# Optimization experiments

Hardware: AMD Instinct MI355X
Metric: run time of the kernel (lower is better)

Reference implementation:

```python
import jax, jax.numpy as jnp
import numpy as np

D_INPUT = 1024
N_HEADS = 16
D_INNER = 64
SEQ = 1024
PREV = 1024
BS = 4
LN_EPS = 1e-5


def _rel_shift(x):
    # x: (i, j, b, h) -> Transformer-XL relative shift trick
    i, j, b, h = x.shape
    zero_pad = jnp.zeros((i, 1, b, h), dtype=x.dtype)
    return jnp.concatenate([zero_pad, x], axis=1).reshape(j + 1, i, b, h)[1:].reshape(i, j, b, h)


def setup_inputs() -> dict:
    key = jax.random.key(0)
    ks = jax.random.split(key, 9)
    w = 0.02
    return {
        "input_": jax.random.normal(ks[0], (SEQ, BS, D_INPUT), jnp.float32),
        "pos_embs": jax.random.normal(ks[1], (SEQ + PREV, D_INPUT), jnp.float32),
        "memory": jax.random.normal(ks[2], (PREV, BS, D_INPUT), jnp.float32),
        "u": jax.random.normal(ks[3], (N_HEADS, D_INNER), jnp.float32) * w,
        "v": jax.random.normal(ks[4], (N_HEADS, D_INNER), jnp.float32) * w,
        "W_kv": jax.random.normal(ks[5], (D_INPUT, 2 * N_HEADS * D_INNER), jnp.float32) * w,
        "W_q": jax.random.normal(ks[6], (D_INPUT, N_HEADS * D_INNER), jnp.float32) * w,
        "W_p": jax.random.normal(ks[7], (D_INPUT, N_HEADS * D_INNER), jnp.float32) * w,
        "W_out": jax.random.normal(ks[8], (N_HEADS * D_INNER, D_INPUT), jnp.float32) * w,
        "ln_g": jnp.ones((D_INPUT,), jnp.float32),
        "ln_b": jnp.zeros((D_INPUT,), jnp.float32),
    }


def reference(input_, pos_embs, memory, u, v, W_kv, W_q, W_p, W_out, ln_g, ln_b):
    S, B, D = input_.shape
    P = memory.shape[0]
    T = S + P
    H, d = u.shape
    scale = 1.0 / (d ** 0.5)

    x_mem = jnp.concatenate([memory, input_], axis=0)          # (T, B, D)
    kv = x_mem @ W_kv                                          # (T, B, 2*H*d)
    k, val = jnp.split(kv, 2, axis=-1)
    k = k.reshape(T, B, H, d)
    val = val.reshape(T, B, H, d)
    q = (input_ @ W_q).reshape(S, B, H, d)                     # (S, B, H, d)

    content_attn = jnp.einsum('ibhd,jbhd->ijbh', q + u, k)     # (S, T, B, H)
    p = (pos_embs @ W_p).reshape(T, H, d)                      # (T, H, d)
    position_attn = jnp.einsum('ibhd,jhd->ijbh', q + v, p)     # (S, T, B, H)
    position_attn = _rel_shift(position_attn)

    attn = jax.nn.softmax((content_attn + position_attn) * scale, axis=1)
    awv = jnp.einsum('ijbh,jbhd->ibhd', attn, val).reshape(S, B, H * d)

    out = input_ + awv @ W_out                                 # residual
    mu = jnp.mean(out, axis=-1, keepdims=True)
    var = jnp.mean(jnp.square(out - mu), axis=-1, keepdims=True)
    return (out - mu) * jax.lax.rsqrt(var + LN_EPS) * ln_g + ln_b
```

## Files before the change

kernel.cpp:

```cpp
#include <hip/hip_runtime.h>
#include <cstdint>
#include <cstddef>

#define S_  1024
#define B_  4
#define T_  2048
#define H_  16

typedef short     short8 __attribute__((ext_vector_type(8)));
typedef float     f32x4  __attribute__((ext_vector_type(4)));
typedef unsigned short u16x8 __attribute__((ext_vector_type(8)));

__device__ __forceinline__ unsigned short f2b(float f){
  uint32_t x = __builtin_bit_cast(uint32_t, f);
  x = (x + 0x7fffu + ((x >> 16) & 1u)) >> 16;
  return (unsigned short)x;
}
__device__ __forceinline__ unsigned short f2bt(float f){
  return (unsigned short)(__builtin_bit_cast(uint32_t, f) >> 16);
}
__device__ __forceinline__ float b2f(unsigned short u){
  return __builtin_bit_cast(float, ((uint32_t)u) << 16);
}

__device__ __forceinline__ void gl_lds16(const unsigned short* g, unsigned short* l){
  __builtin_amdgcn_global_load_lds(
      (const __attribute__((address_space(1))) void*)g,
      (__attribute__((address_space(3))) void*)l,
      16, 0, 0);
}

__global__ __launch_bounds__(256) void cvt_all(
    const float* __restrict__ memsrc, const float* __restrict__ inp,
    const float* __restrict__ pos,
    unsigned short* __restrict__ xb, unsigned short* __restrict__ posb)
{
  int i = (blockIdx.x * 256 + threadIdx.x) * 4;
  const float* src;
  unsigned short* dst;
  if (i < 8192 * 1024){
    src = (i < 4096 * 1024) ? (memsrc + i) : (inp + (i - 4096 * 1024));
    dst = xb + i;
  } else {
    int i2 = i - 8192 * 1024;
    src = pos + i2;
    dst = posb + i2;
  }
  float4 x = *(const float4*)src;
  ushort4 o;
  o.x = f2b(x.x); o.y = f2b(x.y); o.z = f2b(x.z); o.w = f2b(x.w);
  *(ushort4*)dst = o;
}

__global__ __launch_bounds__(256) void wtrans_all(
    const float* __restrict__ Wkv, const float* __restrict__ Wq,
    const float* __restrict__ Wp,  const float* __restrict__ Wout,
    unsigned short* __restrict__ WkvT, unsigned short* __restrict__ WqT,
    unsigned short* __restrict__ WpT,  unsigned short* __restrict__ WoutT)
{
  __shared__ float tile[32][33];
  int blk = blockIdx.x;
  const float* in; unsigned short* out; int C, bx, by;
  if (blk < 2048){ in = Wkv; out = WkvT; C = 2048; bx = blk & 63; by = blk >> 6; }
  else {
    int r = blk - 2048; int wi = r >> 10; r &= 1023;
    C = 1024; bx = r & 31; by = r >> 5;
    in  = (wi == 0) ? Wq  : ((wi == 1) ? Wp  : Wout);
    out = (wi == 0) ? WqT : ((wi == 1) ? WpT : WoutT);
  }
  const int R0 = by * 32, C0 = bx * 32;
  const int t = threadIdx.x;
  const int r = t >> 3, c4 = (t & 7) * 4;
  float4 x = *(const float4*)(in + (size_t)(R0 + r) * C + C0 + c4);
  tile[r][c4+0] = x.x; tile[r][c4+1] = x.y; tile[r][c4+2] = x.z; tile[r][c4+3] = x.w;
  __syncthreads();
  ushort4 o;
  o.x = f2b(tile[c4+0][r]); o.y = f2b(tile[c4+1][r]);
  o.z = f2b(tile[c4+2][r]); o.w = f2b(tile[c4+3][r]);
  *(ushort4*)(out + (size_t)(C0 + r) * 1024 + R0 + c4) = o;
}

__global__ __launch_bounds__(256) void vtrans(
    const unsigned short* __restrict__ kvb, unsigned short* __restrict__ vtg)
{
  __shared__ __align__(16) unsigned short tile[64][72];
  const int t = threadIdx.x;
  const int bh = blockIdx.y;
  const int b = bh >> 4, h = bh & 15;
  const int t0 = blockIdx.x * 64;
  #pragma unroll
  for (int l = 0; l < 2; ++l){
    int idx = t + l * 256;
    int row = idx >> 3, seg = (idx & 7) * 8;
    u16x8 x = *(const u16x8*)(kvb + ((size_t)(t0 + row) * 4 + b) * 2048 + 1024 + h * 64 + seg);
    *(u16x8*)&tile[row][seg] = x;
  }
  __syncthreads();
  #pragma unroll
  for (int l = 0; l < 2; ++l){
    int idx = t + l * 256;
    int d = idx >> 3, nseg = (idx & 7) * 8;
    u16x8 o;
    #pragma unroll
    for (int j = 0; j < 8; ++j) o[j] = tile[nseg + j][d];
    *(u16x8*)(vtg + ((size_t)bh * 64 + d) * 2048 + t0 + nseg) = o;
  }
}

#define AS_IDX(row,k) ((((row) >> 3) * 512) + (((k) >> 3) * 64) + (((row) & 7) * 8) + ((k) & 7))

__global__ __launch_bounds__(256) void gemm_multi(
    const unsigned short* __restrict__ xb,
    const unsigned short* __restrict__ posb,
    const unsigned short* __restrict__ WkvT,
    const unsigned short* __restrict__ WqT,
    const unsigned short* __restrict__ WpT,
    unsigned short* __restrict__ kvb,
    unsigned short* __restrict__ qbb,
    unsigned short* __restrict__ pbb)
{
  const unsigned short *A, *BT;
  unsigned short* C;
  int N, local;
  int bx = (blockIdx.x & 7) * 176 + (blockIdx.x >> 3);
  if (bx < 1024){       A = xb;                       BT = WkvT; C = kvb; N = 2048; local = bx;        }
  else if (bx < 1280){  A = xb + (size_t)4096 * 1024; BT = WqT;  C = qbb; N = 1024; local = bx - 1024; }
  else {                A = posb;                     BT = WpT;  C = pbb; N = 1024; local = bx - 1280; }
  const int nb = N >> 7;
  const int M0 = (local / nb) * 128, N0 = (local % nb) * 128;
  const int K = 1024;

  __shared__ __align__(16) unsigned short As[128 * 64];
  __shared__ __align__(16) unsigned short Bs[128 * 64];
  const int t = threadIdx.x;
  const int w = t >> 6, lane = t & 63, quad = lane >> 4, l16 = lane & 15;
  const int wm = (w >> 1) * 64, wn = (w & 1) * 64;
  const int lr = lane & 7, lcb = lane >> 3;

  f32x4 acc[4][4] = {};

  for (int k0 = 0; k0 < K; k0 += 64){
    __syncthreads();
    #pragma unroll
    for (int i = 0; i < 4; ++i){
      int blk = 4 * w + i;
      gl_lds16(A  + (size_t)(M0 + 8 * blk + lr) * K + k0 + lcb * 8, As + blk * 512);
      gl_lds16(BT + (size_t)(N0 + 8 * blk + lr) * K + k0 + lcb * 8, Bs + blk * 512);
    }
    __syncthreads();
    #pragma unroll
    for (int ks = 0; ks < 2; ++ks){
      short8 af[4], bf[4];
      #pragma unroll
      for (int rt = 0; rt < 4; ++rt)
        af[rt] = *(short8*)&As[AS_IDX(wm + rt * 16 + l16, ks * 32 + quad * 8)];
      #pragma unroll
      for (int ct = 0; ct < 4; ++ct)
        bf[ct] = *(short8*)&Bs[AS_IDX(wn + ct * 16 + l16, ks * 32 + quad * 8)];
      #pragma unroll
      for (int rt = 0; rt < 4; ++rt)
        #pragma unroll
        for (int ct = 0; ct < 4; ++ct)
          acc[rt][ct] = __builtin_amdgcn_mfma_f32_16x16x32_bf16(af[rt], bf[ct], acc[rt][ct], 0, 0, 0);
    }
  }

  #pragma unroll
  for (int rt = 0; rt < 4; ++rt)
    #pragma unroll
    for (int r = 0; r < 4; ++r){
      int row = M0 + wm + rt * 16 + quad * 4 + r;
      #pragma unroll
      for (int ct = 0; ct < 4; ++ct)
        C[(size_t)row * N + N0 + wn + ct * 16 + l16] = f2b(acc[rt][ct][r]);
    }
}

__global__ __launch_bounds__(256) void gemm_outk(
    const unsigned short* __restrict__ A,
    const unsigned short* __restrict__ BT,
    float* __restrict__ OutP)
{
  const int K = 1024, N = 1024;
  int lid = blockIdx.x + 8 * (blockIdx.y + 32 * blockIdx.z);
  int sw  = (lid & 7) * 64 + (lid >> 3);
  const int N0 = (sw & 7) * 128;
  const int M0 = ((sw >> 3) & 31) * 128;
  const int kz = sw >> 8;
  const int k0s = kz * 512, k0e = k0s + 512;
  float* outF = OutP + (size_t)kz * 4096 * 1024;

  __shared__ __align__(16) unsigned short As[128 * 64];
  __shared__ __align__(16) unsigned short Bs[128 * 64];
  const int t = threadIdx.x;
  const int w = t >> 6, lane = t & 63, quad = lane >> 4, l16 = lane & 15;
  const int wm = (w >> 1) * 64, wn = (w & 1) * 64;
  const int lr = lane & 7, lcb = lane >> 3;

  f32x4 acc[4][4] = {};

  for (int k0 = k0s; k0 < k0e; k0 += 64){
    __syncthreads();
    #pragma unroll
    for (int i = 0; i < 4; ++i){
      int blk = 4 * w + i;
      gl_lds16(A  + (size_t)(M0 + 8 * blk + lr) * K + k0 + lcb * 8, As + blk * 512);
      gl_lds16(BT + (size_t)(N0 + 8 * blk + lr) * K + k0 + lcb * 8, Bs + blk * 512);
    }
    __syncthreads();
    #pragma unroll
    for (int ks = 0; ks < 2; ++ks){
      short8 af[4], bf[4];
      #pragma unroll
      for (int rt = 0; rt < 4; ++rt)
        af[rt] = *(short8*)&As[AS_IDX(wm + rt * 16 + l16, ks * 32 + quad * 8)];
      #pragma unroll
      for (int ct = 0; ct < 4; ++ct)
        bf[ct] = *(short8*)&Bs[AS_IDX(wn + ct * 16 + l16, ks * 32 + quad * 8)];
      #pragma unroll
      for (int rt = 0; rt < 4; ++rt)
        #pragma unroll
        for (int ct = 0; ct < 4; ++ct)
          acc[rt][ct] = __builtin_amdgcn_mfma_f32_16x16x32_bf16(af[rt], bf[ct], acc[rt][ct], 0, 0, 0);
    }
  }

  #pragma unroll
  for (int rt = 0; rt < 4; ++rt)
    #pragma unroll
    for (int r = 0; r < 4; ++r){
      int row = M0 + wm + rt * 16 + quad * 4 + r;
      #pragma unroll
      for (int ct = 0; ct < 4; ++ct)
        outF[(size_t)row * N + N0 + wn + ct * 16 + l16] = acc[rt][ct][r];
    }
}

#define SP_IX(gm,n) ((gm) * 64 + ((n) ^ (((gm) & 12) << 2)))

__global__ __launch_bounds__(256, 3) void attn_mfma(
    const unsigned short* __restrict__ qb,
    const unsigned short* __restrict__ kvb,
    const unsigned short* __restrict__ pbm,
    const unsigned short* __restrict__ vtg,
    const float* __restrict__ ub, const float* __restrict__ vb,
    unsigned short* __restrict__ opart,
    float* __restrict__ lpart)
{
  __shared__ __align__(16) unsigned short Kc[64 * 64];
  __shared__ __align__(16) unsigned short VT[64 * 64];
  __shared__ __align__(16) unsigned short Pw[128 * 64];
  __shared__ __align__(16) unsigned short SP[64 * 64];

  const int t = threadIdx.x;
  const int i0 = blockIdx.x * 64;
  const int bh = blockIdx.y;
  const int jh = blockIdx.z;
  const int b = bh >> 4, h = bh & 15;
  const int w = t >> 6, lane = t & 63, quad = lane >> 4, l16 = lane & 15;
  const int colbase = h * 64 + quad * 8;
  const int ctLo = 3 - w;

  const float SCQ = 0.1803368801f;
  const float EOF_ = 23.0831206f;

  short8 qu[2], qv[2][2];
  #pragma unroll
  for (int cs = 0; cs < 2; ++cs){
    int gr = i0 + 16 * w + l16 + cs;
    #pragma unroll
    for (int ks = 0; ks < 2; ++ks){
      u16x8 q8 = *(const u16x8*)(qb + ((size_t)gr * 4 + b) * 1024 + colbase + ks * 32);
      #pragma unroll
      for (int j = 0; j < 8; ++j){
        float f = b2f(q8[j]);
        qv[cs][ks][j] = (short)f2b((f + vb[colbase + ks * 32 + j]) * SCQ);
        if (cs == 0) qu[ks][j] = (short)f2b((f + ub[colbase + ks * 32 + j]) * SCQ);
      }
    }
  }

  f32x4 oacc[4] = {};
  float lsum[4] = {0.f, 0.f, 0.f, 0.f};

  u16x8 pk[2], pv2[2], pp[4];

  auto loadKV = [&](int jc){
    const int j0 = jc * 64;
    #pragma unroll
    for (int l = 0; l < 2; ++l){
      int idx = t + l * 256;
      int row = idx >> 3, cb = idx & 7;
      pk[l]  = *(const u16x8*)(kvb + ((size_t)(j0 + row) * 4 + b) * 2048 + h * 64 + cb * 8);
      pv2[l] = *(const u16x8*)(vtg + ((size_t)bh * 64 + row) * 2048 + j0 + cb * 8);
    }
  };

  auto loadPPfull = [&](int jc){
    const int D = jc * 64 - i0;
    #pragma unroll
    for (int l = 0; l < 4; ++l){
      int idx = t + l * 256;
      int row = idx >> 3, cb = idx & 7;
      int pr;
      if (D <= 960)          pr = D + 960 + row;
      else if (D == 1024)    pr = (row < 64) ? (1984 + row) : (row - 65);
      else                   pr = D - 1089 + row;
      u16x8 x;
      if (pr >= 0 && pr < T_){
        x = *(const u16x8*)(pbm + (size_t)pr * 1024 + h * 64 + cb * 8);
      } else {
        for (int j = 0; j < 8; ++j) x[j] = 0;
      }
      pp[l] = x;
    }
  };

  auto loadPPhalf = [&](int jc){
    const int D = jc * 64 - i0;
    #pragma unroll
    for (int l = 0; l < 2; ++l){
      int idx = t + l * 256;
      int rowh = idx >> 3, cb = idx & 7;
      int pr = (D <= 960) ? (D + 1024 + rowh) : (D - 1025 + rowh);
      u16x8 x;
      if (pr >= 0 && pr < T_){
        x = *(const u16x8*)(pbm + (size_t)pr * 1024 + h * 64 + cb * 8);
      } else {
        for (int j = 0; j < 8; ++j) x[j] = 0;
      }
      pp[l] = x;
    }
  };

  auto storeKV = [&](){
    #pragma unroll
    for (int l = 0; l < 2; ++l){
      int idx = t + l * 256;
      int row = idx >> 3, cb = idx & 7;
      int sw = (cb ^ (row & 7)) * 8;
      *(u16x8*)&Kc[row * 64 + sw] = pk[l];
      *(u16x8*)&VT[row * 64 + sw] = pv2[l];
    }
  };
  auto storePPfull = [&](){
    #pragma unroll
    for (int l = 0; l < 4; ++l){
      int idx = t + l * 256;
      int row = idx >> 3, cb = idx & 7;
      *(u16x8*)&Pw[row * 64 + ((cb ^ (row & 7)) * 8)] = pp[l];
    }
  };
  auto storePPhalf = [&](int physh){
    #pragma unroll
    for (int l = 0; l < 2; ++l){
      int idx = t + l * 256;
      int rowh = idx >> 3, cb = idx & 7;
      *(u16x8*)&Pw[(physh * 64 + rowh) * 64 + ((cb ^ (rowh & 7)) * 8)] = pp[l];
    }
  };

  const int jcs = jh * 16, jce = jcs + 16;
  loadKV(jcs);
  loadPPfull(jcs);
  int par = 0;

  #pragma unroll 1
  for (int jc = jcs; jc < jce; ++jc){
    const int D = jc * 64 - i0;

    __syncthreads();
    storeKV();
    if (jc == jcs) storePPfull(); else storePPhalf(1 ^ par);
    if (jc + 1 < jce){ loadKV(jc + 1); loadPPhalf(jc + 1); }
    __syncthreads();

    #pragma unroll
    for (int ci = 0; ci < 5; ++ci){
      int ct = ctLo + ci;
      int cs = (D <= 960) ? 0 : ((D >= 1088) ? 1 : ((ct >= 4) ? 1 : 0));
      f32x4 racc = {};
      #pragma unroll
      for (int ks = 0; ks < 2; ++ks){
        int rr = ct * 16 + l16;
        int prow = ((rr >> 6) ^ par) * 64 + (rr & 63);
        short8 bf = *(short8*)&Pw[prow * 64 + (((ks * 4 + quad) ^ (rr & 7)) * 8)];
        racc = __builtin_amdgcn_mfma_f32_16x16x32_bf16(qv[cs][ks], bf, racc, 0, 0, 0);
      }
      int c = ct * 16 + l16;
      #pragma unroll
      for (int r = 0; r < 4; ++r){
        int gm = 16 * w + quad * 4 + r;
        int n = c + gm - 63;
        if ((unsigned)n < 64u) SP[SP_IX(gm, n)] = f2bt(racc[r]);
      }
    }

    f32x4 cacc[4] = {};
    #pragma unroll
    for (int ks = 0; ks < 2; ++ks){
      #pragma unroll
      for (int ct = 0; ct < 4; ++ct){
        int rr = ct * 16 + l16;
        short8 bf = *(short8*)&Kc[rr * 64 + (((ks * 4 + quad) ^ (rr & 7)) * 8)];
        cacc[ct] = __builtin_amdgcn_mfma_f32_16x16x32_bf16(qu[ks], bf, cacc[ct], 0, 0, 0);
      }
    }

    #pragma unroll
    for (int ct = 0; ct < 4; ++ct){
      #pragma unroll
      for (int r = 0; r < 4; ++r){
        int gm = 16 * w + quad * 4 + r;
        int n = ct * 16 + l16;
        int ix = SP_IX(gm, n);
        float s = cacc[ct][r] + b2f(SP[ix]);
        float e = __builtin_amdgcn_exp2f(s - EOF_);
        lsum[r] += e;
        SP[ix] = f2bt(e);
      }
    }

    #pragma unroll
    for (int ks = 0; ks < 2; ++ks){
      short8 af = *(short8*)&SP[SP_IX(16 * w + l16, ks * 32 + quad * 8)];
      #pragma unroll
      for (int dt = 0; dt < 4; ++dt){
        int rr = dt * 16 + l16;
        short8 bf = *(short8*)&VT[rr * 64 + (((ks * 4 + quad) ^ (rr & 7)) * 8)];
        oacc[dt] = __builtin_amdgcn_mfma_f32_16x16x32_bf16(af, bf, oacc[dt], 0, 0, 0);
      }
    }

    par ^= 1;
  }

  unsigned short* ob = opart + (size_t)jh * 4096 * 1024;
  float* lb = lpart + (size_t)jh * 4096 * 16;
  #pragma unroll
  for (int r = 0; r < 4; ++r){
    float red = lsum[r];
    #pragma unroll
    for (int mk = 1; mk < 16; mk <<= 1)
      red += __shfl_xor(red, mk, 64);
    int srow = i0 + 16 * w + quad * 4 + r;
    int grow = srow * 4 + b;
    #pragma unroll
    for (int dt = 0; dt < 4; ++dt)
      ob[(size_t)grow * 1024 + h * 64 + dt * 16 + l16] = f2bt(oacc[dt][r]);
    if (l16 == 0) lb[(size_t)grow * 16 + h] = red;
  }
}

__global__ __launch_bounds__(256) void attn_combine(
    const unsigned short* __restrict__ opart, const float* __restrict__ lpart,
    unsigned short* __restrict__ awvb)
{
  const int grow = blockIdx.x, t = threadIdx.x;
  const int d4 = t * 4, h = t >> 4;
  float l = lpart[(size_t)grow * 16 + h] + lpart[(size_t)4096 * 16 + grow * 16 + h];
  float inv = 1.f / l;
  ushort4 a = *(const ushort4*)(opart + (size_t)grow * 1024 + d4);
  ushort4 c = *(const ushort4*)(opart + (size_t)4096 * 1024 + grow * 1024 + d4);
  ushort4 o;
  o.x = f2bt((b2f(a.x) + b2f(c.x)) * inv);
  o.y = f2bt((b2f(a.y) + b2f(c.y)) * inv);
  o.z = f2bt((b2f(a.z) + b2f(c.z)) * inv);
  o.w = f2bt((b2f(a.w) + b2f(c.w)) * inv);
  *(ushort4*)(awvb + (size_t)grow * 1024 + d4) = o;
}

__global__ __launch_bounds__(256) void ln2_kernel(
    const float* __restrict__ inp, const float* __restrict__ OutP,
    const float* __restrict__ g, const float* __restrict__ bb,
    float* __restrict__ out)
{
  const int row = blockIdx.x, t = threadIdx.x;
  float4 x  = *(const float4*)(inp  + (size_t)row * 1024 + t * 4);
  float4 p0 = *(const float4*)(OutP + (size_t)row * 1024 + t * 4);
  float4 p1 = *(const float4*)(OutP + (size_t)4096 * 1024 + row * 1024 + t * 4);
  x.x += p0.x + p1.x; x.y += p0.y + p1.y; x.z += p0.z + p1.z; x.w += p0.w + p1.w;
  float s  = x.x + x.y + x.z + x.w;
  float s2 = x.x*x.x + x.y*x.y + x.z*x.z + x.w*x.w;
  #pragma unroll
  for (int o = 32; o > 0; o >>= 1){
    s  += __shfl_down(s, o);
    s2 += __shfl_down(s2, o);
  }
  __shared__ float rs[4], rs2[4];
  int w = t >> 6, lane = t & 63;
  if (lane == 0){ rs[w] = s; rs2[w] = s2; }
  __syncthreads();
  s  = rs[0] + rs[1] + rs[2] + rs[3];
  s2 = rs2[0] + rs2[1] + rs2[2] + rs2[3];
  float mu   = s * (1.f/1024.f);
  float var  = s2 * (1.f/1024.f) - mu*mu;
  float rstd = rsqrtf(var + 1e-5f);
  float4 gg = *(const float4*)(g + t*4);
  float4 bv = *(const float4*)(bb + t*4);
  float4 o;
  o.x = (x.x - mu)*rstd*gg.x + bv.x;
  o.y = (x.y - mu)*rstd*gg.y + bv.y;
  o.z = (x.z - mu)*rstd*gg.z + bv.z;
  o.w = (x.w - mu)*rstd*gg.w + bv.w;
  *(float4*)(out + (size_t)row * 1024 + t * 4) = o;
}

extern "C" void kernel_launch(void* const* d_in, const int* in_sizes, int n_in,
                              void* d_out, int out_size, void* d_ws, size_t ws_size,
                              hipStream_t stream) {
  (void)in_sizes; (void)n_in; (void)out_size; (void)ws_size;
  const float* input_ = (const float*)d_in[0];
  const float* pos    = (const float*)d_in[1];
  const float* mem    = (const float*)d_in[2];
  const float* u      = (const float*)d_in[3];
  const float* v      = (const float*)d_in[4];
  const float* Wkv    = (const float*)d_in[5];
  const float* Wq     = (const float*)d_in[6];
  const float* Wp     = (const float*)d_in[7];
  const float* Wout   = (const float*)d_in[8];
  const float* lng    = (const float*)d_in[9];
  const float* lnb    = (const float*)d_in[10];
  float* out = (float*)d_out;

  unsigned short* ws   = (unsigned short*)d_ws;
  unsigned short* xb    = ws;
  unsigned short* posb  = xb    + (size_t)8192*1024;
  unsigned short* WkvT  = posb  + (size_t)2048*1024;
  unsigned short* WqT   = WkvT  + (size_t)2048*1024;
  unsigned short* WpT   = WqT   + (size_t)1024*1024;
  unsigned short* WoutT = WpT   + (size_t)1024*1024;
  unsigned short* kvb   = WoutT + (size_t)1024*1024;
  unsigned short* qbb   = kvb   + (size_t)8192*2048;
  unsigned short* pbb   = qbb   + (size_t)4096*1024;
  unsigned short* vtg   = pbb   + (size_t)2048*1024;
  unsigned short* awvb  = vtg   + (size_t)4096*2048;

  unsigned short* opart = xb;
  float*          lpart = (float*)posb;
  float*          OutP  = (float*)kvb;

  cvt_all<<<10240, 256, 0, stream>>>(mem, input_, pos, xb, posb);
  wtrans_all<<<5120, 256, 0, stream>>>(Wkv, Wq, Wp, Wout, WkvT, WqT, WpT, WoutT);

  gemm_multi<<<1408, 256, 0, stream>>>(xb, posb, WkvT, WqT, WpT, kvb, qbb, pbb);

  vtrans<<<dim3(32, 64), 256, 0, stream>>>(kvb, vtg);

  attn_mfma<<<dim3(16, 64, 2), 256, 0, stream>>>(qbb, kvb, pbb, vtg, u, v, opart, lpart);
  attn_combine<<<4096, 256, 0, stream>>>(opart, lpart, awvb);

  gemm_outk<<<dim3(8, 32, 2), 256, 0, stream>>>(awvb, WoutT, OutP);
  ln2_kernel<<<4096, 256, 0, stream>>>(input_, OutP, lng, lnb, out);
}
```

Baseline: 403.3 us.

## Pre-swizzle V into MFMA fragment layout and load directly to registers

The V transpose kernel now writes V in the exact per-lane MFMA B-fragment order, so the attention kernel loads each wave's V fragments straight from global memory into registers. This removes the VT shared-memory tile, its stores and its LDS reads, which reduces LDS usage per block. In exchange, every wave loads the full V fragment set separately (4x redundant global/L2 traffic per block), and these loads are issued at the top of each iteration, adding register pressure.

```diff
diff --git a/kernel.cpp b/kernel.cpp
--- a/kernel.cpp
+++ b/kernel.cpp
@@ -80,30 +80,32 @@
   *(ushort4*)(out + (size_t)(C0 + r) * 1024 + R0 + c4) = o;
 }
 
-__global__ __launch_bounds__(256) void vtrans(
-    const unsigned short* __restrict__ kvb, unsigned short* __restrict__ vtg)
-{
-  __shared__ __align__(16) unsigned short tile[64][72];
+__global__ __launch_bounds__(256) void vfrag(
+    const unsigned short* __restrict__ kvb, unsigned short* __restrict__ vfg)
+{
+  __shared__ __align__(16) unsigned short tileV[64][72];
   const int t = threadIdx.x;
+  const int jc = blockIdx.x;
   const int bh = blockIdx.y;
   const int b = bh >> 4, h = bh & 15;
-  const int t0 = blockIdx.x * 64;
   #pragma unroll
   for (int l = 0; l < 2; ++l){
     int idx = t + l * 256;
-    int row = idx >> 3, seg = (idx & 7) * 8;
-    u16x8 x = *(const u16x8*)(kvb + ((size_t)(t0 + row) * 4 + b) * 2048 + 1024 + h * 64 + seg);
-    *(u16x8*)&tile[row][seg] = x;
+    int tr = idx >> 3, seg = (idx & 7) * 8;
+    u16x8 x = *(const u16x8*)(kvb + ((size_t)(jc * 64 + tr) * 4 + b) * 2048 + 1024 + h * 64 + seg);
+    *(u16x8*)&tileV[tr][seg] = x;
   }
   __syncthreads();
   #pragma unroll
   for (int l = 0; l < 2; ++l){
-    int idx = t + l * 256;
-    int d = idx >> 3, nseg = (idx & 7) * 8;
+    int u = t + l * 256;
+    int f = u >> 6, lane = u & 63;
+    int ks = f >> 2, dt = f & 3;
+    int quad = lane >> 4, l16 = lane & 15;
     u16x8 o;
     #pragma unroll
-    for (int j = 0; j < 8; ++j) o[j] = tile[nseg + j][d];
-    *(u16x8*)(vtg + ((size_t)bh * 64 + d) * 2048 + t0 + nseg) = o;
+    for (int j = 0; j < 8; ++j) o[j] = tileV[ks * 32 + quad * 8 + j][dt * 16 + l16];
+    *(u16x8*)(vfg + (((size_t)bh * 32 + jc) * 8 + f) * 512 + lane * 8) = o;
   }
 }
 
@@ -242,13 +244,12 @@
     const unsigned short* __restrict__ qb,
     const unsigned short* __restrict__ kvb,
     const unsigned short* __restrict__ pbm,
-    const unsigned short* __restrict__ vtg,
+    const unsigned short* __restrict__ vfg,
     const float* __restrict__ ub, const float* __restrict__ vb,
     unsigned short* __restrict__ opart,
     float* __restrict__ lpart)
 {
   __shared__ __align__(16) unsigned short Kc[64 * 64];
-  __shared__ __align__(16) unsigned short VT[64 * 64];
   __shared__ __align__(16) unsigned short Pw[128 * 64];
   __shared__ __align__(16) unsigned short SP[64 * 64];
 
@@ -283,16 +284,15 @@
   f32x4 oacc[4] = {};
   float lsum[4] = {0.f, 0.f, 0.f, 0.f};
 
-  u16x8 pk[2], pv2[2], pp[4];
-
-  auto loadKV = [&](int jc){
+  u16x8 pk[2], pp[4];
+
+  auto loadK = [&](int jc){
     const int j0 = jc * 64;
     #pragma unroll
     for (int l = 0; l < 2; ++l){
       int idx = t + l * 256;
       int row = idx >> 3, cb = idx & 7;
-      pk[l]  = *(const u16x8*)(kvb + ((size_t)(j0 + row) * 4 + b) * 2048 + h * 64 + cb * 8);
-      pv2[l] = *(const u16x8*)(vtg + ((size_t)bh * 64 + row) * 2048 + j0 + cb * 8);
+      pk[l] = *(const u16x8*)(kvb + ((size_t)(j0 + row) * 4 + b) * 2048 + h * 64 + cb * 8);
     }
   };
 
@@ -333,14 +333,12 @@
     }
   };
 
-  auto storeKV = [&](){
+  auto storeK = [&](){
     #pragma unroll
     for (int l = 0; l < 2; ++l){
       int idx = t + l * 256;
       int row = idx >> 3, cb = idx & 7;
-      int sw = (cb ^ (row & 7)) * 8;
-      *(u16x8*)&Kc[row * 64 + sw] = pk[l];
-      *(u16x8*)&VT[row * 64 + sw] = pv2[l];
+      *(u16x8*)&Kc[row * 64 + ((cb ^ (row & 7)) * 8)] = pk[l];
     }
   };
   auto storePPfull = [&](){
@@ -361,7 +359,7 @@
   };
 
   const int jcs = jh * 16, jce = jcs + 16;
-  loadKV(jcs);
+  loadK(jcs);
   loadPPfull(jcs);
   int par = 0;
 
@@ -369,10 +367,18 @@
   for (int jc = jcs; jc < jce; ++jc){
     const int D = jc * 64 - i0;
 
+    const unsigned short* vB = vfg + (((size_t)bh * 32 + jc) * 8) * 512 + lane * 8;
+    short8 vf[2][4];
+    #pragma unroll
+    for (int ks = 0; ks < 2; ++ks)
+      #pragma unroll
+      for (int dt = 0; dt < 4; ++dt)
+        vf[ks][dt] = *(const short8*)(vB + (ks * 4 + dt) * 512);
+
     __syncthreads();
-    storeKV();
+    storeK();
     if (jc == jcs) storePPfull(); else storePPhalf(1 ^ par);
-    if (jc + 1 < jce){ loadKV(jc + 1); loadPPhalf(jc + 1); }
+    if (jc + 1 < jce){ loadK(jc + 1); loadPPhalf(jc + 1); }
     __syncthreads();
 
     #pragma unroll
@@ -425,11 +431,8 @@
     for (int ks = 0; ks < 2; ++ks){
       short8 af = *(short8*)&SP[SP_IX(16 * w + l16, ks * 32 + quad * 8)];
       #pragma unroll
-      for (int dt = 0; dt < 4; ++dt){
-        int rr = dt * 16 + l16;
-        short8 bf = *(short8*)&VT[rr * 64 + (((ks * 4 + quad) ^ (rr & 7)) * 8)];
-        oacc[dt] = __builtin_amdgcn_mfma_f32_16x16x32_bf16(af, bf, oacc[dt], 0, 0, 0);
-      }
+      for (int dt = 0; dt < 4; ++dt)
+        oacc[dt] = __builtin_amdgcn_mfma_f32_16x16x32_bf16(af, vf[ks][dt], oacc[dt], 0, 0, 0);
     }
 
     par ^= 1;
@@ -533,8 +536,8 @@
   unsigned short* kvb   = WoutT + (size_t)1024*1024;
   unsigned short* qbb   = kvb   + (size_t)8192*2048;
   unsigned short* pbb   = qbb   + (size_t)4096*1024;
-  unsigned short* vtg   = pbb   + (size_t)2048*1024;
-  unsigned short* awvb  = vtg   + (size_t)4096*2048;
+  unsigned short* vfg   = pbb   + (size_t)2048*1024;
+  unsigned short* awvb  = vfg   + (size_t)4096*2048;
 
   unsigned short* opart = xb;
   float*          lpart = (float*)posb;
@@ -545,9 +548,9 @@
 
   gemm_multi<<<1408, 256, 0, stream>>>(xb, posb, WkvT, WqT, WpT, kvb, qbb, pbb);
 
-  vtrans<<<dim3(32, 64), 256, 0, stream>>>(kvb, vtg);
-
-  attn_mfma<<<dim3(16, 64, 2), 256, 0, stream>>>(qbb, kvb, pbb, vtg, u, v, opart, lpart);
+  vfrag<<<dim3(32, 64), 256, 0, stream>>>(kvb, vfg);
+
+  attn_mfma<<<dim3(16, 64, 2), 256, 0, stream>>>(qbb, kvb, pbb, vfg, u, v, opart, lpart);
   attn_combine<<<4096, 256, 0, stream>>>(opart, lpart, awvb);
 
   gemm_outk<<<dim3(8, 32, 2), 256, 0, stream>>>(awvb, WoutT, OutP);
```

Result: slower. 523.5 us (+29.8%).
